# Performance work log

Hardware: AMD Instinct MI355X
Metric: run time of the kernel (lower is better)

The kernel has to match this reference:

```python
import jax, jax.numpy as jnp
import numpy as np

N = 50000
E = 1600000
H, C = 4, 32
NEG_SLOPE = 0.2
EPS = 1e-16


def _l2norm_row(a):
    # F.normalize(a, p=2, dim=1) for a of shape [1, F]
    return a / jnp.maximum(jnp.linalg.norm(a, axis=1, keepdims=True), 1e-12)


def setup_inputs() -> dict:
    key = jax.random.key(0)
    ks = jax.random.split(key, 7)
    x = jax.random.normal(ks[0], (N, 256), dtype=jnp.float32)
    edge_index = jax.random.randint(ks[1], (2, E), 0, N, dtype=jnp.int32)
    v_mapping = jax.random.normal(ks[2], (64, 256), dtype=jnp.float32) * 0.1
    W_src = jax.random.normal(ks[3], (256, H * C), dtype=jnp.float32) * 0.06
    att_src = jax.random.normal(ks[4], (1, 64), dtype=jnp.float32)
    att_dst = jax.random.normal(ks[5], (1, 64), dtype=jnp.float32)
    bias = jnp.zeros((H * C,), dtype=jnp.float32)
    return {"x": x, "edge_index": edge_index, "v_mapping": v_mapping,
            "W_src": W_src, "att_src": att_src, "att_dst": att_dst, "bias": bias}


def reference(x, edge_index, v_mapping, W_src, att_src, att_dst, bias):
    # node projection: [N, H, C]
    x_proj = (x @ W_src).reshape(-1, H, C)
    # attention-locator scores: scalar per node
    score = x @ v_mapping.T                      # [N, F]
    a_src = (score * _l2norm_row(att_src)).sum(-1)  # [N]
    a_dst = (score * _l2norm_row(att_dst)).sum(-1)  # [N]

    src, dst = edge_index[0], edge_index[1]
    alpha = a_src[src] + a_dst[dst]              # [E]
    alpha = jax.nn.leaky_relu(alpha, NEG_SLOPE)
    # segment softmax over destination nodes
    m = jax.ops.segment_max(alpha, dst, num_segments=N)
    alpha = jnp.exp(alpha - jax.lax.stop_gradient(m)[dst])
    denom = jax.ops.segment_sum(alpha, dst, num_segments=N)
    alpha = alpha / (denom[dst] + EPS)           # [E]

    msg = x_proj[src] * alpha[:, None, None]     # [E, H, C]
    agg = jax.ops.segment_sum(msg, dst, num_segments=N)  # [N, H, C]

    out = x_proj + agg                           # residual as in forward
    out = out.reshape(-1, H * C) + bias          # concat heads + bias
    return out
```

## Files before the change

kernel.cpp:

```cpp
#include <hip/hip_runtime.h>

#define N_NODES 50000
#define E_EDGES 1600000
#define HC 128
#define NEG_SLOPE 0.2f
#define SM_EPS 1e-16f
#define NBKT 782
#define BKT_STRIDE 2600
#define EPBH 2048

typedef __attribute__((ext_vector_type(8))) short short8v;
typedef __attribute__((ext_vector_type(4))) float f32x4;

__device__ inline unsigned bf16pack(float a, float b) {
  unsigned ua = __float_as_uint(a), ub = __float_as_uint(b);
  ua = (ua + 0x7fffu + ((ua >> 16) & 1u)) >> 16;
  ub = (ub + 0x7fffu + ((ub >> 16) & 1u)) >> 16;
  return ua | (ub << 16);
}

__global__ __launch_bounds__(256) void k0_init(
    const float* __restrict__ v_mapping,
    const float* __restrict__ att_src,
    const float* __restrict__ att_dst,
    const float* __restrict__ W,
    unsigned short* __restrict__ wT,
    int* __restrict__ gcursor) {
  const int tid = threadIdx.x, bid = blockIdx.x;
  if (bid < 4) {
    const int i = bid * 256 + tid;
    if (i < NBKT) gcursor[i] = i * BKT_STRIDE;
  }

  __shared__ float wv[2][256];
  {
    const int j = tid;
    float ns = 0.f, nd = 0.f;
    for (int f = 0; f < 64; ++f) {
      float a = att_src[f]; ns = fmaf(a, a, ns);
      float b = att_dst[f]; nd = fmaf(b, b, nd);
    }
    ns = fmaxf(sqrtf(ns), 1e-12f);
    nd = fmaxf(sqrtf(nd), 1e-12f);
    float s = 0.f, d = 0.f;
    for (int f = 0; f < 64; ++f) {
      float v = v_mapping[f * 256 + j];
      s = fmaf(v, att_src[f], s);
      d = fmaf(v, att_dst[f], d);
    }
    wv[0][j] = s / ns;
    wv[1][j] = d / nd;
  }
  __syncthreads();

#pragma unroll
  for (int r = 0; r < 8; ++r) {
    const int n = bid * 8 + r;
    const int k = tid;
    float v;
    if (n < 128) v = W[k * 128 + n];
    else if (n == 128) v = wv[0][k];
    else if (n == 129) v = wv[1][k];
    else v = 0.f;
    unsigned u = __float_as_uint(v);
    u = (u + 0x7fffu + ((u >> 16) & 1u)) >> 16;
    wT[n * 256 + k] = (unsigned short)u;
  }
}

__global__ __launch_bounds__(256) void k1_fused(
    const float* __restrict__ x,
    const unsigned short* __restrict__ wT,
    unsigned* __restrict__ xpb,
    float* __restrict__ a_src, float* __restrict__ a_dst,
    const int* __restrict__ ei,
    int* __restrict__ gcursor, unsigned* __restrict__ coarse) {
  __shared__ char smem[64 * 264 * 2];
  const int bid = blockIdx.x;
  const int tid = threadIdx.x;

  if (bid & 1) {
    int* chist = (int*)smem;
    int* gbase = (int*)(smem + 3200);
    int* ccur  = (int*)(smem + 6400);
    const int ebase = (bid >> 1) * EPBH;
    for (int b = tid; b < NBKT; b += 256) { chist[b] = 0; ccur[b] = 0; }
    __syncthreads();

#pragma unroll
    for (int i = 0; i < 8; ++i) {
      const int e = ebase + i * 256 + tid;
      if (e < E_EDGES) atomicAdd(&chist[ei[E_EDGES + e] >> 6], 1);
    }
    __syncthreads();

    for (int b = tid; b < NBKT; b += 256) {
      const int c = chist[b];
      if (c > 0) gbase[b] = atomicAdd(&gcursor[b], c);
    }
    __syncthreads();

#pragma unroll
    for (int i = 0; i < 8; ++i) {
      const int e = ebase + i * 256 + tid;
      if (e < E_EDGES) {
        const int s = ei[e];
        const int d = ei[E_EDGES + e];
        const int b = d >> 6;
        const int pos = gbase[b] + atomicAdd(&ccur[b], 1);
        if (pos < (b + 1) * BKT_STRIDE)
          coarse[pos] = (unsigned)s | ((unsigned)(d & 63) << 16);
      }
    }
    return;
  }

  unsigned short* xs = (unsigned short*)smem;
  const int w = tid >> 6, lane = tid & 63;
  const int rowbase = (bid >> 1) * 64;

  const float4* x4 = (const float4*)x;
#pragma unroll
  for (int c = 0; c < 16; ++c) {
    const int idx = c * 256 + tid;
    const int row = idx >> 6, c4 = idx & 63;
    float4 v = make_float4(0.f, 0.f, 0.f, 0.f);
    if (rowbase + row < N_NODES) v = x4[(size_t)(rowbase + row) * 64 + c4];
    uint2 p;
    p.x = bf16pack(v.x, v.y);
    p.y = bf16pack(v.z, v.w);
    *(uint2*)&xs[row * 264 + c4 * 4] = p;
  }
  __syncthreads();

  f32x4 acc[9];
#pragma unroll
  for (int t = 0; t < 9; ++t) acc[t] = (f32x4){0.f, 0.f, 0.f, 0.f};

  const int m = lane & 15, kq = lane >> 4;
  const unsigned short* arow = &xs[(w * 16 + m) * 264 + kq * 8];
#pragma unroll
  for (int ks = 0; ks < 8; ++ks) {
    const short8v af = *(const short8v*)(arow + ks * 32);
#pragma unroll
    for (int ct = 0; ct < 9; ++ct) {
      const short8v bf = *(const short8v*)(wT + (ct * 16 + m) * 256 + ks * 32 + kq * 8);
      acc[ct] = __builtin_amdgcn_mfma_f32_16x16x32_bf16(af, bf, acc[ct], 0, 0, 0);
    }
  }

  if (m < 2) {
    float* ap = m ? a_dst : a_src;
#pragma unroll
    for (int i = 0; i < 4; ++i) {
      const int rg = rowbase + w * 16 + kq * 4 + i;
      if (rg < N_NODES) ap[rg] = acc[8][i];
    }
  }

  float* cs = (float*)(smem + (size_t)w * 16 * 264 * 2);
#pragma unroll
  for (int ct = 0; ct < 8; ++ct)
#pragma unroll
    for (int i = 0; i < 4; ++i)
      cs[(kq * 4 + i) * 132 + ct * 16 + m] = acc[ct][i];
  __syncthreads();

  const int prow = lane & 15, q = lane >> 4;
  const int grow = rowbase + w * 16 + prow;
  unsigned uu[16];
#pragma unroll
  for (int u = 0; u < 16; ++u) {
    const float2 f2 = *(const float2*)&cs[prow * 132 + q * 32 + u * 2];
    uu[u] = bf16pack(f2.x, f2.y);
  }
  if (grow < N_NODES) {
    uint4* d4 = (uint4*)&xpb[(size_t)grow * 64 + q * 16];
    d4[0] = make_uint4(uu[0], uu[1], uu[2], uu[3]);
    d4[1] = make_uint4(uu[4], uu[5], uu[6], uu[7]);
    d4[2] = make_uint4(uu[8], uu[9], uu[10], uu[11]);
    d4[3] = make_uint4(uu[12], uu[13], uu[14], uu[15]);
  }
}

__global__ __launch_bounds__(512) void kc2_reduce(
    const int* __restrict__ gcursor, const unsigned* __restrict__ coarse,
    const float* __restrict__ a_src, const float* __restrict__ a_dst,
    const unsigned* __restrict__ xpb,
    const float* __restrict__ bias,
    float* __restrict__ out) {
  __shared__ unsigned sorted[BKT_STRIDE];
  __shared__ int hist[64], cur[64];
  __shared__ int base[65];
  __shared__ float adl[64];
  const int b = blockIdx.x;
  const int tid = threadIdx.x;
  const int cstart = b * BKT_STRIDE;
  const int cnt = min(gcursor[b] - cstart, BKT_STRIDE);

  if (tid < 64) {
    hist[tid] = 0; cur[tid] = 0;
    const int dg = (b << 6) | tid;
    adl[tid] = (dg < N_NODES) ? a_dst[dg] : 0.f;
  }
  __syncthreads();

  for (int j = tid; j < cnt; j += 512)
    atomicAdd(&hist[(coarse[cstart + j] >> 16) & 63], 1);
  __syncthreads();

  if (tid < 64) {
    const int h = hist[tid];
    int inc = h;
#pragma unroll
    for (int off = 1; off < 64; off <<= 1) {
      int t = __shfl_up(inc, off);
      if (tid >= off) inc += t;
    }
    base[tid] = inc - h;
    if (tid == 63) base[64] = inc;
  }
  __syncthreads();

  for (int j = tid; j < cnt; j += 512) {
    const unsigned e2 = coarse[cstart + j];
    const int src = e2 & 0xffffu;
    const int dloc = (e2 >> 16) & 63;
    float a = a_src[src] + adl[dloc];
    a = a > 0.f ? a : NEG_SLOPE * a;
    unsigned uev = __float_as_uint(__expf(a));
    uev = (uev + 0x7fffu + ((uev >> 16) & 1u)) >> 16;
    const int p = base[dloc] + atomicAdd(&cur[dloc], 1);
    sorted[p] = (unsigned)src | (uev << 16);
  }
  __syncthreads();

  const int g = tid >> 4, gl = tid & 15;
  const uint4* xp4 = (const uint4*)xpb;
  const float4* br = (const float4*)bias;
  const float4 b0 = br[2 * gl], b1 = br[2 * gl + 1];

  for (int dl = g; dl < 64; dl += 32) {
    const int dst = (b << 6) | dl;
    if (dst >= N_NODES) break;
    const int s0 = base[dl];
    const int cntd = base[dl + 1] - s0;

    float acc[8];
#pragma unroll
    for (int i = 0; i < 8; ++i) acc[i] = 0.f;
    float den = 0.f;

    int j = 0;
    for (; j + 4 <= cntd; j += 4) {
      unsigned u[4];
      float ev[4];
      uint4 v[4];
#pragma unroll
      for (int t = 0; t < 4; ++t) {
        u[t] = sorted[s0 + j + t];
        ev[t] = __uint_as_float(u[t] & 0xffff0000u);
        v[t] = xp4[(size_t)(u[t] & 0xffffu) * 16 + gl];
      }
#pragma unroll
      for (int t = 0; t < 4; ++t) {
        den += ev[t];
        acc[0] = fmaf(ev[t], __uint_as_float(v[t].x << 16), acc[0]);
        acc[1] = fmaf(ev[t], __uint_as_float(v[t].x & 0xffff0000u), acc[1]);
        acc[2] = fmaf(ev[t], __uint_as_float(v[t].y << 16), acc[2]);
        acc[3] = fmaf(ev[t], __uint_as_float(v[t].y & 0xffff0000u), acc[3]);
        acc[4] = fmaf(ev[t], __uint_as_float(v[t].z << 16), acc[4]);
        acc[5] = fmaf(ev[t], __uint_as_float(v[t].z & 0xffff0000u), acc[5]);
        acc[6] = fmaf(ev[t], __uint_as_float(v[t].w << 16), acc[6]);
        acc[7] = fmaf(ev[t], __uint_as_float(v[t].w & 0xffff0000u), acc[7]);
      }
    }
    for (; j < cntd; ++j) {
      const unsigned u = sorted[s0 + j];
      const float ev = __uint_as_float(u & 0xffff0000u);
      const uint4 v = xp4[(size_t)(u & 0xffffu) * 16 + gl];
      den += ev;
      acc[0] = fmaf(ev, __uint_as_float(v.x << 16), acc[0]);
      acc[1] = fmaf(ev, __uint_as_float(v.x & 0xffff0000u), acc[1]);
      acc[2] = fmaf(ev, __uint_as_float(v.y << 16), acc[2]);
      acc[3] = fmaf(ev, __uint_as_float(v.y & 0xffff0000u), acc[3]);
      acc[4] = fmaf(ev, __uint_as_float(v.z << 16), acc[4]);
      acc[5] = fmaf(ev, __uint_as_float(v.z & 0xffff0000u), acc[5]);
      acc[6] = fmaf(ev, __uint_as_float(v.w << 16), acc[6]);
      acc[7] = fmaf(ev, __uint_as_float(v.w & 0xffff0000u), acc[7]);
    }

    const float inv = 1.f / (den + SM_EPS);
    const uint4 ur = xp4[(size_t)dst * 16 + gl];
    float4 o0, o1;
    o0.x = __uint_as_float(ur.x << 16)         + b0.x + acc[0] * inv;
    o0.y = __uint_as_float(ur.x & 0xffff0000u) + b0.y + acc[1] * inv;
    o0.z = __uint_as_float(ur.y << 16)         + b0.z + acc[2] * inv;
    o0.w = __uint_as_float(ur.y & 0xffff0000u) + b0.w + acc[3] * inv;
    o1.x = __uint_as_float(ur.z << 16)         + b1.x + acc[4] * inv;
    o1.y = __uint_as_float(ur.z & 0xffff0000u) + b1.y + acc[5] * inv;
    o1.z = __uint_as_float(ur.w << 16)         + b1.z + acc[6] * inv;
    o1.w = __uint_as_float(ur.w & 0xffff0000u) + b1.w + acc[7] * inv;
    float4* orow = (float4*)(out + (size_t)dst * HC);
    orow[2 * gl] = o0;
    orow[2 * gl + 1] = o1;
  }
}

extern "C" void kernel_launch(void* const* d_in, const int* in_sizes, int n_in,
                              void* d_out, int out_size, void* d_ws, size_t ws_size,
                              hipStream_t stream) {
  const float* x         = (const float*)d_in[0];
  const int*   ei        = (const int*)d_in[1];
  const float* v_mapping = (const float*)d_in[2];
  const float* W_src     = (const float*)d_in[3];
  const float* att_src   = (const float*)d_in[4];
  const float* att_dst   = (const float*)d_in[5];
  const float* bias      = (const float*)d_in[6];
  float* out = (float*)d_out;

  char* ws = (char*)d_ws;
  unsigned*       xpb     = (unsigned*)ws;        ws += (size_t)N_NODES * 64 * 4;
  float*          a_src   = (float*)ws;           ws += (size_t)N_NODES * 4;
  float*          a_dst   = (float*)ws;           ws += (size_t)N_NODES * 4;
  unsigned short* wT      = (unsigned short*)ws;  ws += 144 * 256 * 2;
  int*            gcursor = (int*)ws;             ws += ((NBKT + 127) / 128) * 128 * 4;
  unsigned*       coarse  = (unsigned*)ws;        ws += (size_t)NBKT * BKT_STRIDE * 4;

  k0_init<<<18, 256, 0, stream>>>(v_mapping, att_src, att_dst, W_src, wT, gcursor);
  k1_fused<<<2 * NBKT, 256, 0, stream>>>(x, wT, xpb, a_src, a_dst, ei, gcursor, coarse);
  kc2_reduce<<<NBKT, 512, 0, stream>>>(gcursor, coarse, a_src, a_dst, xpb, bias, out);
}
```

Baseline: 148.8 us.

## Split fused projection/bucketing kernel into separate edge-binning and node-projection kernels

Result: faster. 143.3 us (-3.7%).

```diff
diff --git a/kernel.cpp b/kernel.cpp
--- a/kernel.cpp
+++ b/kernel.cpp
@@ -7,7 +7,8 @@
 #define SM_EPS 1e-16f
 #define NBKT 782
 #define BKT_STRIDE 2600
-#define EPBH 2048
+#define EPB1 3072
+#define NB1 521
 
 typedef __attribute__((ext_vector_type(8))) short short8v;
 typedef __attribute__((ext_vector_type(4))) float f32x4;
@@ -68,56 +69,15 @@
   }
 }
 
-__global__ __launch_bounds__(256) void k1_fused(
+__global__ __launch_bounds__(256) void k1_node(
     const float* __restrict__ x,
     const unsigned short* __restrict__ wT,
     unsigned* __restrict__ xpb,
-    float* __restrict__ a_src, float* __restrict__ a_dst,
-    const int* __restrict__ ei,
-    int* __restrict__ gcursor, unsigned* __restrict__ coarse) {
-  __shared__ char smem[64 * 264 * 2];
-  const int bid = blockIdx.x;
+    float* __restrict__ a_src, float* __restrict__ a_dst) {
+  __shared__ unsigned short xs[64 * 264];
   const int tid = threadIdx.x;
-
-  if (bid & 1) {
-    int* chist = (int*)smem;
-    int* gbase = (int*)(smem + 3200);
-    int* ccur  = (int*)(smem + 6400);
-    const int ebase = (bid >> 1) * EPBH;
-    for (int b = tid; b < NBKT; b += 256) { chist[b] = 0; ccur[b] = 0; }
-    __syncthreads();
-
-#pragma unroll
-    for (int i = 0; i < 8; ++i) {
-      const int e = ebase + i * 256 + tid;
-      if (e < E_EDGES) atomicAdd(&chist[ei[E_EDGES + e] >> 6], 1);
-    }
-    __syncthreads();
-
-    for (int b = tid; b < NBKT; b += 256) {
-      const int c = chist[b];
-      if (c > 0) gbase[b] = atomicAdd(&gcursor[b], c);
-    }
-    __syncthreads();
-
-#pragma unroll
-    for (int i = 0; i < 8; ++i) {
-      const int e = ebase + i * 256 + tid;
-      if (e < E_EDGES) {
-        const int s = ei[e];
-        const int d = ei[E_EDGES + e];
-        const int b = d >> 6;
-        const int pos = gbase[b] + atomicAdd(&ccur[b], 1);
-        if (pos < (b + 1) * BKT_STRIDE)
-          coarse[pos] = (unsigned)s | ((unsigned)(d & 63) << 16);
-      }
-    }
-    return;
-  }
-
-  unsigned short* xs = (unsigned short*)smem;
   const int w = tid >> 6, lane = tid & 63;
-  const int rowbase = (bid >> 1) * 64;
+  const int rowbase = blockIdx.x * 64;
 
   const float4* x4 = (const float4*)x;
 #pragma unroll
@@ -158,7 +118,7 @@
     }
   }
 
-  float* cs = (float*)(smem + (size_t)w * 16 * 264 * 2);
+  float* cs = (float*)&xs[w * 16 * 264];
 #pragma unroll
   for (int ct = 0; ct < 8; ++ct)
 #pragma unroll
@@ -180,6 +140,44 @@
     d4[1] = make_uint4(uu[4], uu[5], uu[6], uu[7]);
     d4[2] = make_uint4(uu[8], uu[9], uu[10], uu[11]);
     d4[3] = make_uint4(uu[12], uu[13], uu[14], uu[15]);
+  }
+}
+
+__global__ __launch_bounds__(1024) void kc1_coarse(
+    const int* __restrict__ ei,
+    int* __restrict__ gcursor, unsigned* __restrict__ coarse) {
+  __shared__ int chist[NBKT];
+  __shared__ int gbase[NBKT];
+  __shared__ int ccur[NBKT];
+  const int tid = threadIdx.x;
+  const int ebase = blockIdx.x * EPB1;
+  for (int b = tid; b < NBKT; b += 1024) { chist[b] = 0; ccur[b] = 0; }
+  __syncthreads();
+
+#pragma unroll
+  for (int i = 0; i < 3; ++i) {
+    const int e = ebase + i * 1024 + tid;
+    if (e < E_EDGES) atomicAdd(&chist[ei[E_EDGES + e] >> 6], 1);
+  }
+  __syncthreads();
+
+  for (int b = tid; b < NBKT; b += 1024) {
+    const int c = chist[b];
+    if (c > 0) gbase[b] = atomicAdd(&gcursor[b], c);
+  }
+  __syncthreads();
+
+#pragma unroll
+  for (int i = 0; i < 3; ++i) {
+    const int e = ebase + i * 1024 + tid;
+    if (e < E_EDGES) {
+      const int s = ei[e];
+      const int d = ei[E_EDGES + e];
+      const int b = d >> 6;
+      const int pos = gbase[b] + atomicAdd(&ccur[b], 1);
+      if (pos < (b + 1) * BKT_STRIDE)
+        coarse[pos] = (unsigned)s | ((unsigned)(d & 63) << 16);
+    }
   }
 }
 
@@ -328,6 +326,7 @@
   unsigned*       coarse  = (unsigned*)ws;        ws += (size_t)NBKT * BKT_STRIDE * 4;
 
   k0_init<<<18, 256, 0, stream>>>(v_mapping, att_src, att_dst, W_src, wT, gcursor);
-  k1_fused<<<2 * NBKT, 256, 0, stream>>>(x, wT, xpb, a_src, a_dst, ei, gcursor, coarse);
+  kc1_coarse<<<NB1, 1024, 0, stream>>>(ei, gcursor, coarse);
+  k1_node<<<(N_NODES + 63) / 64, 256, 0, stream>>>(x, wT, xpb, a_src, a_dst);
   kc2_reduce<<<NBKT, 512, 0, stream>>>(gcursor, coarse, a_src, a_dst, xpb, bias, out);
 }
```

## Load GEMM A-fragments directly to registers and shrink LDS, rebalance hist blocks

Applied to the files above, without the earlier changes.

New measurement: 127.0 us. 14.7% less time.

```diff
diff --git a/kernel.cpp b/kernel.cpp
--- a/kernel.cpp
+++ b/kernel.cpp
@@ -7,10 +7,14 @@
 #define SM_EPS 1e-16f
 #define NBKT 782
 #define BKT_STRIDE 2600
-#define EPBH 2048
+#define EPB1 3072
+#define NB_GEMM 782
+#define NB_HIST 521
 
 typedef __attribute__((ext_vector_type(8))) short short8v;
 typedef __attribute__((ext_vector_type(4))) float f32x4;
+
+union U8 { uint4 u; short8v s; };
 
 __device__ inline unsigned bf16pack(float a, float b) {
   unsigned ua = __float_as_uint(a), ub = __float_as_uint(b);
@@ -75,20 +79,23 @@
     float* __restrict__ a_src, float* __restrict__ a_dst,
     const int* __restrict__ ei,
     int* __restrict__ gcursor, unsigned* __restrict__ coarse) {
-  __shared__ char smem[64 * 264 * 2];
+  __shared__ char smem[17408];
   const int bid = blockIdx.x;
   const int tid = threadIdx.x;
-
-  if (bid & 1) {
+  const int r5 = bid % 5, q5 = bid / 5;
+
+  if (r5 >= 3) {
+    const int hid = q5 * 2 + (r5 - 3);
+    if (hid >= NB_HIST) return;
     int* chist = (int*)smem;
     int* gbase = (int*)(smem + 3200);
     int* ccur  = (int*)(smem + 6400);
-    const int ebase = (bid >> 1) * EPBH;
+    const int ebase = hid * EPB1;
     for (int b = tid; b < NBKT; b += 256) { chist[b] = 0; ccur[b] = 0; }
     __syncthreads();
 
 #pragma unroll
-    for (int i = 0; i < 8; ++i) {
+    for (int i = 0; i < 12; ++i) {
       const int e = ebase + i * 256 + tid;
       if (e < E_EDGES) atomicAdd(&chist[ei[E_EDGES + e] >> 6], 1);
     }
@@ -101,7 +108,7 @@
     __syncthreads();
 
 #pragma unroll
-    for (int i = 0; i < 8; ++i) {
+    for (int i = 0; i < 12; ++i) {
       const int e = ebase + i * 256 + tid;
       if (e < E_EDGES) {
         const int s = ei[e];
@@ -115,37 +122,36 @@
     return;
   }
 
-  unsigned short* xs = (unsigned short*)smem;
+  const int gid = q5 * 3 + r5;
+  if (gid >= NB_GEMM) return;
   const int w = tid >> 6, lane = tid & 63;
-  const int rowbase = (bid >> 1) * 64;
-
-  const float4* x4 = (const float4*)x;
-#pragma unroll
-  for (int c = 0; c < 16; ++c) {
-    const int idx = c * 256 + tid;
-    const int row = idx >> 6, c4 = idx & 63;
-    float4 v = make_float4(0.f, 0.f, 0.f, 0.f);
-    if (rowbase + row < N_NODES) v = x4[(size_t)(rowbase + row) * 64 + c4];
-    uint2 p;
-    p.x = bf16pack(v.x, v.y);
-    p.y = bf16pack(v.z, v.w);
-    *(uint2*)&xs[row * 264 + c4 * 4] = p;
-  }
-  __syncthreads();
+  const int rowbase = gid * 64;
+  const int m = lane & 15, kq = lane >> 4;
+
+  const int arow_idx = rowbase + w * 16 + m;
+  const int arow_c = arow_idx < N_NODES ? arow_idx : N_NODES - 1;
+  const float4* xr = (const float4*)(x + (size_t)arow_c * 256);
+  short8v af[8];
+#pragma unroll
+  for (int ks = 0; ks < 8; ++ks) {
+    const float4 p0 = xr[kq * 2 + ks * 8];
+    const float4 p1 = xr[kq * 2 + ks * 8 + 1];
+    U8 t;
+    t.u = make_uint4(bf16pack(p0.x, p0.y), bf16pack(p0.z, p0.w),
+                     bf16pack(p1.x, p1.y), bf16pack(p1.z, p1.w));
+    af[ks] = t.s;
+  }
 
   f32x4 acc[9];
 #pragma unroll
   for (int t = 0; t < 9; ++t) acc[t] = (f32x4){0.f, 0.f, 0.f, 0.f};
 
-  const int m = lane & 15, kq = lane >> 4;
-  const unsigned short* arow = &xs[(w * 16 + m) * 264 + kq * 8];
 #pragma unroll
   for (int ks = 0; ks < 8; ++ks) {
-    const short8v af = *(const short8v*)(arow + ks * 32);
 #pragma unroll
     for (int ct = 0; ct < 9; ++ct) {
       const short8v bf = *(const short8v*)(wT + (ct * 16 + m) * 256 + ks * 32 + kq * 8);
-      acc[ct] = __builtin_amdgcn_mfma_f32_16x16x32_bf16(af, bf, acc[ct], 0, 0, 0);
+      acc[ct] = __builtin_amdgcn_mfma_f32_16x16x32_bf16(af[ks], bf, acc[ct], 0, 0, 0);
     }
   }
 
@@ -158,28 +164,29 @@
     }
   }
 
-  float* cs = (float*)(smem + (size_t)w * 16 * 264 * 2);
-#pragma unroll
-  for (int ct = 0; ct < 8; ++ct)
-#pragma unroll
-    for (int i = 0; i < 4; ++i)
-      cs[(kq * 4 + i) * 132 + ct * 16 + m] = acc[ct][i];
-  __syncthreads();
-
+  float* cs = (float*)smem + w * 1088;
   const int prow = lane & 15, q = lane >> 4;
-  const int grow = rowbase + w * 16 + prow;
-  unsigned uu[16];
-#pragma unroll
-  for (int u = 0; u < 16; ++u) {
-    const float2 f2 = *(const float2*)&cs[prow * 132 + q * 32 + u * 2];
-    uu[u] = bf16pack(f2.x, f2.y);
-  }
-  if (grow < N_NODES) {
-    uint4* d4 = (uint4*)&xpb[(size_t)grow * 64 + q * 16];
-    d4[0] = make_uint4(uu[0], uu[1], uu[2], uu[3]);
-    d4[1] = make_uint4(uu[4], uu[5], uu[6], uu[7]);
-    d4[2] = make_uint4(uu[8], uu[9], uu[10], uu[11]);
-    d4[3] = make_uint4(uu[12], uu[13], uu[14], uu[15]);
+  const int growp = rowbase + w * 16 + prow;
+#pragma unroll
+  for (int half = 0; half < 2; ++half) {
+#pragma unroll
+    for (int ct = 0; ct < 4; ++ct)
+#pragma unroll
+      for (int i = 0; i < 4; ++i)
+        cs[(kq * 4 + i) * 68 + ct * 16 + m] = acc[half * 4 + ct][i];
+    __syncthreads();
+    unsigned uu[8];
+#pragma unroll
+    for (int u2 = 0; u2 < 8; ++u2) {
+      const float2 f2 = *(const float2*)&cs[prow * 68 + q * 16 + u2 * 2];
+      uu[u2] = bf16pack(f2.x, f2.y);
+    }
+    if (growp < N_NODES) {
+      uint4* d4 = (uint4*)&xpb[(size_t)growp * 64 + half * 32 + q * 8];
+      d4[0] = make_uint4(uu[0], uu[1], uu[2], uu[3]);
+      d4[1] = make_uint4(uu[4], uu[5], uu[6], uu[7]);
+    }
+    __syncthreads();
   }
 }
 
@@ -328,6 +335,6 @@
   unsigned*       coarse  = (unsigned*)ws;        ws += (size_t)NBKT * BKT_STRIDE * 4;
 
   k0_init<<<18, 256, 0, stream>>>(v_mapping, att_src, att_dst, W_src, wT, gcursor);
-  k1_fused<<<2 * NBKT, 256, 0, stream>>>(x, wT, xpb, a_src, a_dst, ei, gcursor, coarse);
+  k1_fused<<<1305, 256, 0, stream>>>(x, wT, xpb, a_src, a_dst, ei, gcursor, coarse);
   kc2_reduce<<<NBKT, 512, 0, stream>>>(gcursor, coarse, a_src, a_dst, xpb, bias, out);
 }
```
